# Performance work log

Measured on AMD Instinct MI355X. Metric: run time of the kernel, lower is better.

## Reference

```python
import jax, jax.numpy as jnp
import numpy as np

BS = 256      # number of graphs
NODES = 128   # nodes per graph (equal-size segments)
N = BS * NODES
D = 64        # node feature dim
C = 64        # codebook atoms
K = 32        # support points per atom


def setup_inputs() -> dict:
    key = jax.random.key(0)
    k1, k2 = jax.random.split(key)
    x = jax.random.normal(k1, (N, D), dtype=jnp.float32)
    atoms = jax.random.normal(k2, (C, K, D), dtype=jnp.float32)
    batch = jnp.repeat(jnp.arange(BS, dtype=jnp.int64), NODES)  # sorted graph ids
    return {"x": x, "atoms": atoms, "batch": batch, "bs": BS}


def _sq_dists(a, b):
    # a: [..., n, D], b: [..., m, D] -> [..., n, m] squared euclidean distances
    an = jnp.sum(a * a, axis=-1)
    bn = jnp.sum(b * b, axis=-1)
    ab = jnp.einsum('...nd,...md->...nm', a, b)
    return an[..., :, None] + bn[..., None, :] - 2.0 * ab


def reference(x, atoms, batch, bs):
    # Faithful vectorized version of GINSWDSingleModel._mmd_distances with
    # gamma = 1/D (default). Assumes equal-size graphs (batch = repeat(arange(bs), n)).
    Nn, Dd = x.shape
    Cc, Kk, _ = atoms.shape
    n = Nn // bs
    gamma = 1.0 / Dd
    xg = x.reshape(bs, n, Dd)                      # [bs, n, D]

    # k_xx: within-graph RBF kernel mean, per graph -> [bs]
    k_xx = jnp.exp(-gamma * _sq_dists(xg, xg)).mean(axis=(1, 2))

    # k_yy: within-atom kernel mean, per atom -> [C]
    k_yy = jnp.exp(-gamma * _sq_dists(atoms, atoms)).mean(axis=(1, 2))

    # k_xy: cross kernel mean between graph nodes and atom points -> [bs, C]
    xn = jnp.sum(xg * xg, axis=-1)                 # [bs, n]
    an = jnp.sum(atoms * atoms, axis=-1)           # [C, K]
    xa = jnp.einsum('bnd,ckd->bnck', xg, atoms)    # [bs, n, C, K]
    dxy = xn[:, :, None, None] + an[None, None, :, :] - 2.0 * xa
    k_xy = jnp.exp(-gamma * dxy).mean(axis=(1, 3))  # [bs, C]

    return k_xx[:, None] + k_yy[None, :] - 2.0 * k_xy
```

## Files before the change

### kernel.cpp

```cpp
#include <hip/hip_runtime.h>
#include <hip/hip_bf16.h>


constexpr int   NODES = 128;
constexpr int   DD    = 64;
constexpr int   CC    = 64;
constexpr int   KK    = 32;
constexpr float GAMMA = 1.0f / 64.0f;
constexpr float LOG2E = 1.4426950408889634f;
constexpr float C1    = 2.0f * GAMMA * LOG2E;
constexpr float GL    = GAMMA * LOG2E;

typedef __attribute__((ext_vector_type(8)))  short short8;
typedef __attribute__((ext_vector_type(16))) float f32x16;

#define MFMA(a, b, c) __builtin_amdgcn_mfma_f32_32x32x16_bf16((a), (b), (c), 0, 0, 0)

__device__ __forceinline__ float fexp2(float x) {
#if __has_builtin(__builtin_amdgcn_exp2f)
    return __builtin_amdgcn_exp2f(x);
#else
    return exp2f(x);
#endif
}

__device__ __forceinline__ unsigned short f2bf(float f) {
    union { float f; unsigned int u; } a; a.f = f;
    unsigned int u = a.u;
    return (unsigned short)((u + 0x7FFFu + ((u >> 16) & 1u)) >> 16);
}

__device__ __forceinline__ void gl16(const void* g, void* l) {
    __builtin_amdgcn_global_load_lds(
        (const __attribute__((address_space(1))) char*)g,
        (__attribute__((address_space(3))) char*)l, 16, 0, 0);
}

__global__ __launch_bounds__(256) void prep(const float* __restrict__ x,
                                            const float* __restrict__ atoms,
                                            short8* __restrict__ xfrag,
                                            float* __restrict__ nrm,
                                            short8* __restrict__ bfrag,
                                            float* __restrict__ can,
                                            float* __restrict__ kyy) {
    __shared__ float smem[NODES * (DD + 1)];
    const int bid = blockIdx.x, t = threadIdx.x;

    if (bid < 256) {
        const int b = bid;
        float (*a)[DD + 1] = (float(*)[DD + 1])smem;

        const float4* xg = reinterpret_cast<const float4*>(x + (size_t)b * NODES * DD);
        for (int i = t; i < NODES * DD / 4; i += 256) {
            const float4 v = xg[i];
            const int r = i >> 4, c4 = (i & 15) * 4;
            a[r][c4 + 0] = v.x; a[r][c4 + 1] = v.y;
            a[r][c4 + 2] = v.z; a[r][c4 + 3] = v.w;
        }
        __syncthreads();

        if (t < NODES) {
            float s = 0.f;
#pragma unroll
            for (int d = 0; d < DD; ++d) s = fmaf(a[t][d], a[t][d], s);
            nrm[b * NODES + t] = -GL * s;
        }
#pragma unroll
        for (int j = 0; j < 4; ++j) {
            const int e = t + 256 * j;
            const int l = e & 63, sl = e >> 6;
            const int row = (sl >> 2) * 32 + (l & 31);
            const int k0  = (sl & 3) * 16 + (l >> 5) * 8;
            short8 h;
#pragma unroll
            for (int q = 0; q < 8; ++q) h[q] = (short)f2bf(a[row][k0 + q]);
            xfrag[(size_t)b * 1024 + e] = h;
        }
    } else {
        const int c = bid - 256;
        float (*a)[DD + 1] = (float(*)[DD + 1])smem;
        float* an   = smem + KK * (DD + 1);
        float* wred = an + KK;

        const float* ac = atoms + (size_t)c * KK * DD;
        for (int i = t; i < KK * DD; i += 256) a[i >> 6][i & 63] = ac[i];
        __syncthreads();

        if (t < KK) {
            float s = 0.f;
#pragma unroll
            for (int d = 0; d < DD; ++d) s = fmaf(a[t][d], a[t][d], s);
            an[t] = s;
            can[c * KK + t] = -GL * s;
        }
        __syncthreads();

        {
            const int wv = t >> 6, l = t & 63;
            const int kp = l & 31, khh = l >> 5;
            short8 h;
#pragma unroll
            for (int j = 0; j < 8; ++j)
                h[j] = (short)f2bf(C1 * a[kp][wv * 16 + khh * 8 + j]);
            bfrag[(size_t)c * 256 + wv * 64 + l] = h;
        }

        {
            const int i = t >> 3, j0 = (t & 7) * 4;
            float s0 = 0, s1 = 0, s2 = 0, s3 = 0;
            for (int d = 0; d < DD; ++d) {
                const float aid = a[i][d];
                s0 = fmaf(aid, a[j0 + 0][d], s0);
                s1 = fmaf(aid, a[j0 + 1][d], s1);
                s2 = fmaf(aid, a[j0 + 2][d], s2);
                s3 = fmaf(aid, a[j0 + 3][d], s3);
            }
            const float ani = an[i];
            float s = fexp2(-GL * (ani + an[j0 + 0] - 2.f * s0))
                    + fexp2(-GL * (ani + an[j0 + 1] - 2.f * s1))
                    + fexp2(-GL * (ani + an[j0 + 2] - 2.f * s2))
                    + fexp2(-GL * (ani + an[j0 + 3] - 2.f * s3));
#pragma unroll
            for (int off = 32; off; off >>= 1) s += __shfl_xor(s, off);
            if ((t & 63) == 0) wred[t >> 6] = s;
        }
        __syncthreads();
        if (t == 0) kyy[c] = (wred[0] + wred[1] + wred[2] + wred[3]) * (1.0f / (KK * KK));
    }
}

__global__ __launch_bounds__(256, 4) void mmd_fused(const short8* __restrict__ xfrag,
                                                    const short8* __restrict__ bfrag,
                                                    const float* __restrict__ nrm,
                                                    const float* __restrict__ can,
                                                    float* __restrict__ kxxp,
                                                    float* __restrict__ sxyw) {
    const int bid = blockIdx.x, b = bid >> 2, cq = bid & 3;
    const int t = threadIdx.x, w = t >> 6, l = t & 63;
    const int l31 = l & 31, kh = l >> 5;

    __shared__ short8 Bb[2][4][256];
    __shared__ float  part16[4][17][16];

    const short8* xa = xfrag + (size_t)b * 1024;
    short8 A[4];
#pragma unroll
    for (int kt = 0; kt < 4; ++kt) A[kt] = xa[(w * 4 + kt) * 64 + l];

    f32x16 cx;
    {
        const float* nb = nrm + b * NODES + w * 32 + 4 * kh;
#pragma unroll
        for (int q = 0; q < 4; ++q) {
            const float4 v = *reinterpret_cast<const float4*>(nb + 8 * q);
            cx[4*q+0] = v.x; cx[4*q+1] = v.y; cx[4*q+2] = v.z; cx[4*q+3] = v.w;
        }
    }
    float cav[16];
#pragma unroll
    for (int j = 0; j < 16; ++j) cav[j] = can[(cq * 16 + j) * KK + l31];

    const float ec0 = fexp2(nrm[b * NODES + cq * 32 + l31]);
    const short8* bq = bfrag + (size_t)(cq * 16) * 256;

    {
        const short8* src = (w == 0) ? (xa + cq * 256) : (bq + (size_t)(w - 1) * 256);
#pragma unroll
        for (int q = 0; q < 4; ++q) gl16(src + q * 64 + l, &Bb[0][w][q * 64]);
    }
    __syncthreads();

#pragma unroll
    for (int s = 0; s < 5; ++s) {
        if (s < 4) {
            const int g = 4 * (s + 1) + w;
            if (g <= 16) {
                const short8* src = bq + (size_t)(g - 1) * 256;
#pragma unroll
                for (int q = 0; q < 4; ++q)
                    gl16(src + q * 64 + l, &Bb[(s + 1) & 1][w][q * 64]);
            }
        }
#pragma unroll
        for (int p = 0; p < 4; ++p) {
            const int g = 4 * s + p;
            if (g <= 16) {
                short8 Bt[4];
#pragma unroll
                for (int kt = 0; kt < 4; ++kt) Bt[kt] = Bb[s & 1][p][kt * 64 + l];

                float ssum;
                if (g == 0) {
                    f32x16 acc = {};
#pragma unroll
                    for (int kt = 0; kt < 4; ++kt) acc = MFMA(A[kt], Bt[kt], acc);
                    float sa = 0.f, sb = 0.f;
#pragma unroll
                    for (int r = 0; r < 16; r += 2) {
                        sa += fexp2(fmaf(C1, acc[r],     cx[r]));
                        sb += fexp2(fmaf(C1, acc[r + 1], cx[r + 1]));
                    }
                    ssum = (sa + sb) * ec0;
                } else {
                    f32x16 acc;
#pragma unroll
                    for (int r = 0; r < 16; ++r) acc[r] = cx[r] + cav[g - 1];
#pragma unroll
                    for (int kt = 0; kt < 4; ++kt) acc = MFMA(A[kt], Bt[kt], acc);
                    float sa = 0.f, sb = 0.f;
#pragma unroll
                    for (int r = 0; r < 16; r += 2) {
                        sa += fexp2(acc[r]);
                        sb += fexp2(acc[r + 1]);
                    }
                    ssum = sa + sb;
                }
                ssum += __shfl_xor(ssum, 32);
                ssum += __shfl_xor(ssum, 16);
                if (l < 16) part16[w][g][l] = ssum;
            }
        }
        __syncthreads();
    }

    {
        const int o = t >> 4, g = t & 15;
        float s = part16[0][o + 1][g] + part16[1][o + 1][g]
                + part16[2][o + 1][g] + part16[3][o + 1][g];
        s += __shfl_xor(s, 8);
        s += __shfl_xor(s, 4);
        s += __shfl_xor(s, 2);
        s += __shfl_xor(s, 1);
        if (g == 0) sxyw[b * CC + cq * 16 + o] = s;
    }
    if (t < 16) {
        float s = part16[0][0][t] + part16[1][0][t]
                + part16[2][0][t] + part16[3][0][t];
        s += __shfl_xor(s, 8);
        s += __shfl_xor(s, 4);
        s += __shfl_xor(s, 2);
        s += __shfl_xor(s, 1);
        if (t == 0) kxxp[b * 4 + cq] = s;
    }
}

__global__ __launch_bounds__(256) void combine(const float* __restrict__ kxxp,
                                               const float* __restrict__ kyy,
                                               const float* __restrict__ sxyw,
                                               float* __restrict__ out) {
    const int idx = blockIdx.x * 256 + threadIdx.x;
    const int b = idx >> 6, c = idx & 63;
    const float kxx = (kxxp[b * 4 + 0] + kxxp[b * 4 + 1] +
                       kxxp[b * 4 + 2] + kxxp[b * 4 + 3]) * (1.0f / 16384.0f);
    out[idx] = kxx + kyy[c] - sxyw[idx] * (1.0f / 2048.0f);
}

extern "C" void kernel_launch(void* const* d_in, const int* in_sizes, int n_in,
                              void* d_out, int out_size, void* d_ws, size_t ws_size,
                              hipStream_t stream) {
    const float* x     = (const float*)d_in[0];
    const float* atoms = (const float*)d_in[1];
    float* out = (float*)d_out;

    char* ws = (char*)d_ws;
    short8* xfrag = (short8*)(ws);
    short8* bfrag = (short8*)(ws + 4194304);
    float*  nrm   = (float*) (ws + 4456448);
    float*  can   = (float*) (ws + 4587520);
    float*  kyy   = (float*) (ws + 4595712);
    float*  kxxp  = (float*) (ws + 4595968);
    float*  sxyw  = (float*) (ws + 4600064);

    prep      <<<dim3(320),  dim3(256), 0, stream>>>(x, atoms, xfrag, nrm, bfrag, can, kyy);
    mmd_fused <<<dim3(1024), dim3(256), 0, stream>>>(xfrag, bfrag, nrm, can, kxxp, sxyw);
    combine   <<<dim3(CC),   dim3(256), 0, stream>>>(kxxp, kyy, sxyw, out);
}
```

Measured before the change: 29.62 us.

## Fuse x preprocessing and final combine into main MMD kernel

```diff
diff --git a/kernel.cpp b/kernel.cpp
--- a/kernel.cpp
+++ b/kernel.cpp
@@ -36,223 +36,197 @@
         (__attribute__((address_space(3))) char*)l, 16, 0, 0);
 }
 
-__global__ __launch_bounds__(256) void prep(const float* __restrict__ x,
-                                            const float* __restrict__ atoms,
-                                            short8* __restrict__ xfrag,
-                                            float* __restrict__ nrm,
-                                            short8* __restrict__ bfrag,
-                                            float* __restrict__ can,
-                                            float* __restrict__ kyy) {
-    __shared__ float smem[NODES * (DD + 1)];
-    const int bid = blockIdx.x, t = threadIdx.x;
-
-    if (bid < 256) {
-        const int b = bid;
-        float (*a)[DD + 1] = (float(*)[DD + 1])smem;
-
-        const float4* xg = reinterpret_cast<const float4*>(x + (size_t)b * NODES * DD);
-        for (int i = t; i < NODES * DD / 4; i += 256) {
-            const float4 v = xg[i];
-            const int r = i >> 4, c4 = (i & 15) * 4;
-            a[r][c4 + 0] = v.x; a[r][c4 + 1] = v.y;
-            a[r][c4 + 2] = v.z; a[r][c4 + 3] = v.w;
-        }
-        __syncthreads();
-
-        if (t < NODES) {
-            float s = 0.f;
-#pragma unroll
-            for (int d = 0; d < DD; ++d) s = fmaf(a[t][d], a[t][d], s);
-            nrm[b * NODES + t] = -GL * s;
-        }
-#pragma unroll
-        for (int j = 0; j < 4; ++j) {
-            const int e = t + 256 * j;
-            const int l = e & 63, sl = e >> 6;
-            const int row = (sl >> 2) * 32 + (l & 31);
-            const int k0  = (sl & 3) * 16 + (l >> 5) * 8;
-            short8 h;
-#pragma unroll
-            for (int q = 0; q < 8; ++q) h[q] = (short)f2bf(a[row][k0 + q]);
-            xfrag[(size_t)b * 1024 + e] = h;
-        }
-    } else {
-        const int c = bid - 256;
-        float (*a)[DD + 1] = (float(*)[DD + 1])smem;
-        float* an   = smem + KK * (DD + 1);
-        float* wred = an + KK;
-
-        const float* ac = atoms + (size_t)c * KK * DD;
-        for (int i = t; i < KK * DD; i += 256) a[i >> 6][i & 63] = ac[i];
-        __syncthreads();
-
-        if (t < KK) {
-            float s = 0.f;
-#pragma unroll
-            for (int d = 0; d < DD; ++d) s = fmaf(a[t][d], a[t][d], s);
-            an[t] = s;
-            can[c * KK + t] = -GL * s;
-        }
-        __syncthreads();
-
-        {
-            const int wv = t >> 6, l = t & 63;
-            const int kp = l & 31, khh = l >> 5;
-            short8 h;
-#pragma unroll
-            for (int j = 0; j < 8; ++j)
-                h[j] = (short)f2bf(C1 * a[kp][wv * 16 + khh * 8 + j]);
-            bfrag[(size_t)c * 256 + wv * 64 + l] = h;
-        }
-
-        {
-            const int i = t >> 3, j0 = (t & 7) * 4;
-            float s0 = 0, s1 = 0, s2 = 0, s3 = 0;
-            for (int d = 0; d < DD; ++d) {
-                const float aid = a[i][d];
-                s0 = fmaf(aid, a[j0 + 0][d], s0);
-                s1 = fmaf(aid, a[j0 + 1][d], s1);
-                s2 = fmaf(aid, a[j0 + 2][d], s2);
-                s3 = fmaf(aid, a[j0 + 3][d], s3);
-            }
-            const float ani = an[i];
-            float s = fexp2(-GL * (ani + an[j0 + 0] - 2.f * s0))
-                    + fexp2(-GL * (ani + an[j0 + 1] - 2.f * s1))
-                    + fexp2(-GL * (ani + an[j0 + 2] - 2.f * s2))
-                    + fexp2(-GL * (ani + an[j0 + 3] - 2.f * s3));
-#pragma unroll
-            for (int off = 32; off; off >>= 1) s += __shfl_xor(s, off);
-            if ((t & 63) == 0) wred[t >> 6] = s;
-        }
-        __syncthreads();
-        if (t == 0) kyy[c] = (wred[0] + wred[1] + wred[2] + wred[3]) * (1.0f / (KK * KK));
-    }
-}
-
-__global__ __launch_bounds__(256, 4) void mmd_fused(const short8* __restrict__ xfrag,
+__global__ __launch_bounds__(256) void prep_atoms(const float* __restrict__ atoms,
+                                                  short8* __restrict__ bfrag,
+                                                  float* __restrict__ can,
+                                                  float* __restrict__ kyy) {
+    const int c = blockIdx.x, t = threadIdx.x;
+    __shared__ float a[KK][DD + 1];
+    __shared__ float an[KK];
+    __shared__ float wred[4];
+
+    const float* ac = atoms + (size_t)c * KK * DD;
+    for (int i = t; i < KK * DD; i += 256) a[i >> 6][i & 63] = ac[i];
+    __syncthreads();
+
+    if (t < KK) {
+        float s = 0.f;
+#pragma unroll
+        for (int d = 0; d < DD; ++d) s = fmaf(a[t][d], a[t][d], s);
+        an[t] = s;
+        can[c * KK + t] = -GL * s;
+    }
+    __syncthreads();
+
+    {
+        const int wv = t >> 6, l = t & 63;
+        const int kp = l & 31, khh = l >> 5;
+        short8 h;
+#pragma unroll
+        for (int j = 0; j < 8; ++j)
+            h[j] = (short)f2bf(C1 * a[kp][wv * 16 + khh * 8 + j]);
+        bfrag[(size_t)c * 256 + wv * 64 + l] = h;
+    }
+
+    {
+        const int i = t >> 3, j0 = (t & 7) * 4;
+        float s0 = 0, s1 = 0, s2 = 0, s3 = 0;
+        for (int d = 0; d < DD; ++d) {
+            const float aid = a[i][d];
+            s0 = fmaf(aid, a[j0 + 0][d], s0);
+            s1 = fmaf(aid, a[j0 + 1][d], s1);
+            s2 = fmaf(aid, a[j0 + 2][d], s2);
+            s3 = fmaf(aid, a[j0 + 3][d], s3);
+        }
+        const float ani = an[i];
+        float s = fexp2(-GL * (ani + an[j0 + 0] - 2.f * s0))
+                + fexp2(-GL * (ani + an[j0 + 1] - 2.f * s1))
+                + fexp2(-GL * (ani + an[j0 + 2] - 2.f * s2))
+                + fexp2(-GL * (ani + an[j0 + 3] - 2.f * s3));
+#pragma unroll
+        for (int off = 32; off; off >>= 1) s += __shfl_xor(s, off);
+        if ((t & 63) == 0) wred[t >> 6] = s;
+    }
+    __syncthreads();
+    if (t == 0) kyy[c] = (wred[0] + wred[1] + wred[2] + wred[3]) * (1.0f / (KK * KK));
+}
+
+__global__ __launch_bounds__(256, 4) void mmd_fused(const float* __restrict__ x,
                                                     const short8* __restrict__ bfrag,
-                                                    const float* __restrict__ nrm,
                                                     const float* __restrict__ can,
-                                                    float* __restrict__ kxxp,
-                                                    float* __restrict__ sxyw) {
+                                                    const float* __restrict__ kyy,
+                                                    float* __restrict__ out) {
     const int bid = blockIdx.x, b = bid >> 2, cq = bid & 3;
     const int t = threadIdx.x, w = t >> 6, l = t & 63;
     const int l31 = l & 31, kh = l >> 5;
 
     __shared__ short8 Bb[2][4][256];
-    __shared__ float  part16[4][17][16];
-
-    const short8* xa = xfrag + (size_t)b * 1024;
+    __shared__ float  part16[4][20][16];
+    __shared__ float  nl[NODES];
+    __shared__ float  sxy_s[16];
+    __shared__ float  kxx_s;
+
+    float v[32];
+    {
+        const float* xr = x + ((size_t)(b * NODES + w * 32 + l31)) * DD + kh * 8;
+#pragma unroll
+        for (int kt = 0; kt < 4; ++kt) {
+            const float4 p0 = *reinterpret_cast<const float4*>(xr + kt * 16);
+            const float4 p1 = *reinterpret_cast<const float4*>(xr + kt * 16 + 4);
+            v[kt*8+0]=p0.x; v[kt*8+1]=p0.y; v[kt*8+2]=p0.z; v[kt*8+3]=p0.w;
+            v[kt*8+4]=p1.x; v[kt*8+5]=p1.y; v[kt*8+6]=p1.z; v[kt*8+7]=p1.w;
+        }
+    }
+    float xn = 0.f;
+#pragma unroll
+    for (int i = 0; i < 32; ++i) xn = fmaf(v[i], v[i], xn);
+    xn += __shfl_xor(xn, 32);
+    if (l < 32) nl[w * 32 + l] = -GL * xn;
+
     short8 A[4];
 #pragma unroll
-    for (int kt = 0; kt < 4; ++kt) A[kt] = xa[(w * 4 + kt) * 64 + l];
+    for (int kt = 0; kt < 4; ++kt) {
+        short8 h;
+#pragma unroll
+        for (int j = 0; j < 8; ++j) h[j] = (short)f2bf(v[kt * 8 + j]);
+        A[kt] = h;
+        Bb[0][w][kt * 64 + l] = h;
+    }
+
+    float cav[16];
+#pragma unroll
+    for (int j = 0; j < 16; ++j) cav[j] = can[(cq * 16 + j) * KK + l31];
+
+    __syncthreads();
 
     f32x16 cx;
     {
-        const float* nb = nrm + b * NODES + w * 32 + 4 * kh;
+        const float* nb = &nl[w * 32 + 4 * kh];
 #pragma unroll
         for (int q = 0; q < 4; ++q) {
-            const float4 v = *reinterpret_cast<const float4*>(nb + 8 * q);
-            cx[4*q+0] = v.x; cx[4*q+1] = v.y; cx[4*q+2] = v.z; cx[4*q+3] = v.w;
-        }
-    }
-    float cav[16];
-#pragma unroll
-    for (int j = 0; j < 16; ++j) cav[j] = can[(cq * 16 + j) * KK + l31];
-
-    const float ec0 = fexp2(nrm[b * NODES + cq * 32 + l31]);
+            const float4 vq = *reinterpret_cast<const float4*>(nb + 8 * q);
+            cx[4*q+0] = vq.x; cx[4*q+1] = vq.y; cx[4*q+2] = vq.z; cx[4*q+3] = vq.w;
+        }
+    }
+
     const short8* bq = bfrag + (size_t)(cq * 16) * 256;
-
-    {
-        const short8* src = (w == 0) ? (xa + cq * 256) : (bq + (size_t)(w - 1) * 256);
-#pragma unroll
-        for (int q = 0; q < 4; ++q) gl16(src + q * 64 + l, &Bb[0][w][q * 64]);
-    }
-    __syncthreads();
 
 #pragma unroll
     for (int s = 0; s < 5; ++s) {
         if (s < 4) {
-            const int g = 4 * (s + 1) + w;
-            if (g <= 16) {
-                const short8* src = bq + (size_t)(g - 1) * 256;
-#pragma unroll
-                for (int q = 0; q < 4; ++q)
-                    gl16(src + q * 64 + l, &Bb[(s + 1) & 1][w][q * 64]);
+            const short8* src = bq + (size_t)(s * 4 + w) * 256;
+#pragma unroll
+            for (int q = 0; q < 4; ++q)
+                gl16(src + q * 64 + l, &Bb[(s + 1) & 1][w][q * 64]);
+        }
+#pragma unroll
+        for (int p = 0; p < 4; ++p) {
+            short8 Bt[4];
+#pragma unroll
+            for (int kt = 0; kt < 4; ++kt) Bt[kt] = Bb[s & 1][p][kt * 64 + l];
+
+            float ssum;
+            if (s == 0) {
+                f32x16 acc = {};
+#pragma unroll
+                for (int kt = 0; kt < 4; ++kt) acc = MFMA(A[kt], Bt[kt], acc);
+                const float ec0 = fexp2(nl[p * 32 + l31]);
+                float sa = 0.f, sb = 0.f;
+#pragma unroll
+                for (int r = 0; r < 16; r += 2) {
+                    sa += fexp2(fmaf(C1, acc[r],     cx[r]));
+                    sb += fexp2(fmaf(C1, acc[r + 1], cx[r + 1]));
+                }
+                ssum = (sa + sb) * ec0;
+            } else {
+                const int j = (s - 1) * 4 + p;
+                f32x16 acc;
+#pragma unroll
+                for (int r = 0; r < 16; ++r) acc[r] = cx[r] + cav[j];
+#pragma unroll
+                for (int kt = 0; kt < 4; ++kt) acc = MFMA(A[kt], Bt[kt], acc);
+                float sa = 0.f, sb = 0.f;
+#pragma unroll
+                for (int r = 0; r < 16; r += 2) {
+                    sa += fexp2(acc[r]);
+                    sb += fexp2(acc[r + 1]);
+                }
+                ssum = sa + sb;
             }
-        }
-#pragma unroll
-        for (int p = 0; p < 4; ++p) {
-            const int g = 4 * s + p;
-            if (g <= 16) {
-                short8 Bt[4];
-#pragma unroll
-                for (int kt = 0; kt < 4; ++kt) Bt[kt] = Bb[s & 1][p][kt * 64 + l];
-
-                float ssum;
-                if (g == 0) {
-                    f32x16 acc = {};
-#pragma unroll
-                    for (int kt = 0; kt < 4; ++kt) acc = MFMA(A[kt], Bt[kt], acc);
-                    float sa = 0.f, sb = 0.f;
-#pragma unroll
-                    for (int r = 0; r < 16; r += 2) {
-                        sa += fexp2(fmaf(C1, acc[r],     cx[r]));
-                        sb += fexp2(fmaf(C1, acc[r + 1], cx[r + 1]));
-                    }
-                    ssum = (sa + sb) * ec0;
-                } else {
-                    f32x16 acc;
-#pragma unroll
-                    for (int r = 0; r < 16; ++r) acc[r] = cx[r] + cav[g - 1];
-#pragma unroll
-                    for (int kt = 0; kt < 4; ++kt) acc = MFMA(A[kt], Bt[kt], acc);
-                    float sa = 0.f, sb = 0.f;
-#pragma unroll
-                    for (int r = 0; r < 16; r += 2) {
-                        sa += fexp2(acc[r]);
-                        sb += fexp2(acc[r + 1]);
-                    }
-                    ssum = sa + sb;
-                }
-                ssum += __shfl_xor(ssum, 32);
-                ssum += __shfl_xor(ssum, 16);
-                if (l < 16) part16[w][g][l] = ssum;
-            }
+            ssum += __shfl_xor(ssum, 32);
+            ssum += __shfl_xor(ssum, 16);
+            if (l < 16) part16[w][s * 4 + p][l] = ssum;
         }
         __syncthreads();
     }
 
     {
         const int o = t >> 4, g = t & 15;
-        float s = part16[0][o + 1][g] + part16[1][o + 1][g]
-                + part16[2][o + 1][g] + part16[3][o + 1][g];
-        s += __shfl_xor(s, 8);
-        s += __shfl_xor(s, 4);
-        s += __shfl_xor(s, 2);
-        s += __shfl_xor(s, 1);
-        if (g == 0) sxyw[b * CC + cq * 16 + o] = s;
+        float s1 = part16[0][4 + o][g] + part16[1][4 + o][g]
+                 + part16[2][4 + o][g] + part16[3][4 + o][g];
+        s1 += __shfl_xor(s1, 8);
+        s1 += __shfl_xor(s1, 4);
+        s1 += __shfl_xor(s1, 2);
+        s1 += __shfl_xor(s1, 1);
+        if (g == 0) sxy_s[o] = s1;
     }
     if (t < 16) {
-        float s = part16[0][0][t] + part16[1][0][t]
-                + part16[2][0][t] + part16[3][0][t];
-        s += __shfl_xor(s, 8);
-        s += __shfl_xor(s, 4);
-        s += __shfl_xor(s, 2);
-        s += __shfl_xor(s, 1);
-        if (t == 0) kxxp[b * 4 + cq] = s;
-    }
-}
-
-__global__ __launch_bounds__(256) void combine(const float* __restrict__ kxxp,
-                                               const float* __restrict__ kyy,
-                                               const float* __restrict__ sxyw,
-                                               float* __restrict__ out) {
-    const int idx = blockIdx.x * 256 + threadIdx.x;
-    const int b = idx >> 6, c = idx & 63;
-    const float kxx = (kxxp[b * 4 + 0] + kxxp[b * 4 + 1] +
-                       kxxp[b * 4 + 2] + kxxp[b * 4 + 3]) * (1.0f / 16384.0f);
-    out[idx] = kxx + kyy[c] - sxyw[idx] * (1.0f / 2048.0f);
+        float kx = 0.f;
+#pragma unroll
+        for (int ww = 0; ww < 4; ++ww)
+#pragma unroll
+            for (int q = 0; q < 4; ++q) kx += part16[ww][q][t];
+        kx += __shfl_xor(kx, 8);
+        kx += __shfl_xor(kx, 4);
+        kx += __shfl_xor(kx, 2);
+        kx += __shfl_xor(kx, 1);
+        if (t == 0) kxx_s = kx;
+    }
+    __syncthreads();
+    if (t < 16) {
+        out[(size_t)b * CC + cq * 16 + t] =
+            kxx_s * (1.0f / 16384.0f) + kyy[cq * 16 + t] - sxy_s[t] * (1.0f / 2048.0f);
+    }
 }
 
 extern "C" void kernel_launch(void* const* d_in, const int* in_sizes, int n_in,
@@ -263,15 +237,10 @@
     float* out = (float*)d_out;
 
     char* ws = (char*)d_ws;
-    short8* xfrag = (short8*)(ws);
-    short8* bfrag = (short8*)(ws + 4194304);
-    float*  nrm   = (float*) (ws + 4456448);
-    float*  can   = (float*) (ws + 4587520);
-    float*  kyy   = (float*) (ws + 4595712);
-    float*  kxxp  = (float*) (ws + 4595968);
-    float*  sxyw  = (float*) (ws + 4600064);
-
-    prep      <<<dim3(320),  dim3(256), 0, stream>>>(x, atoms, xfrag, nrm, bfrag, can, kyy);
-    mmd_fused <<<dim3(1024), dim3(256), 0, stream>>>(xfrag, bfrag, nrm, can, kxxp, sxyw);
-    combine   <<<dim3(CC),   dim3(256), 0, stream>>>(kxxp, kyy, sxyw, out);
-}
+    short8* bfrag = (short8*)(ws);
+    float*  can   = (float*) (ws + 262144);
+    float*  kyy   = (float*) (ws + 270336);
+
+    prep_atoms<<<dim3(CC),   dim3(256), 0, stream>>>(atoms, bfrag, can, kyy);
+    mmd_fused <<<dim3(1024), dim3(256), 0, stream>>>(x, bfrag, can, kyy, out);
+}
```

Result: no change. 29.37 us (-0.9%).
